# Kernel optimization log

Measured on AMD Instinct MI355X. Metric: run time of the kernel, lower is better.

Reference implementation:

```python
import jax, jax.numpy as jnp
import numpy as np

N_ATOMS = 6144
BOX = 40.0  # Angstrom, simulation box edge


def setup_inputs() -> dict:
    key = jax.random.key(0)
    k1, k2 = jax.random.split(key)
    coordinates = jax.random.uniform(k1, (1, N_ATOMS, 3), dtype=jnp.float32) * BOX
    species = jax.random.randint(k2, (1, N_ATOMS), 0, 4)  # no -1 dummy atoms
    return {"species": species, "coordinates": coordinates, "cutoff": 5}


def reference(species, coordinates, cutoff):
    # Faithful math of CellList.forward with pbc=None (no PBC):
    # the grid/bucket pipeline only accelerates finding all (i, j), i > j
    # pairs with |r_i - r_j| <= cutoff (tril_indices ordering), excluding
    # dummy atoms (species == -1). Output: dense masked distance map where
    # entry [i, j] = distance if pair is a screened neighbor else 0.
    coords = coordinates.reshape(-1, 3)
    n = coords.shape[0]
    cutoff = jnp.float32(cutoff)
    diff = coords[:, None, :] - coords[None, :, :]           # [N, N, 3] = r_i - r_j
    sq = jnp.sum(diff * diff, axis=-1)                       # [N, N]
    dist = jnp.sqrt(jnp.where(sq > 0, sq, 1.0))              # safe sqrt (diag sq==0)
    dummy = species.reshape(-1) == -1
    valid = jnp.tril(jnp.ones((n, n), dtype=bool), k=-1)     # i > j, as tril_indices(offset=-1)
    valid = valid & (~dummy[:, None]) & (~dummy[None, :])
    # screening uses detached coords in the original -> mask is non-diff anyway
    mask = valid & (dist <= cutoff) & (sq > 0)
    return jnp.where(mask, dist, 0.0)
```

## Files before the change

kernel.cpp:

```cpp
#include <hip/hip_runtime.h>
#include <math.h>


constexpr int N     = 6144;
constexpr int CPT   = 8;
constexpr int BLOCK = 256;
constexpr int CPB   = BLOCK * CPT;

template <bool ICHECK>
__device__ __forceinline__ void compute_strip(
    const float* __restrict__ coords, const int* __restrict__ species,
    float T, int i, int j0, float* __restrict__ outp)
{
    const float xi = coords[3 * i + 0];
    const float yi = coords[3 * i + 1];
    const float zi = coords[3 * i + 2];

    const float4* cj = reinterpret_cast<const float4*>(coords + 3 * (size_t)j0);
    float f[24];
#pragma unroll
    for (int q = 0; q < 6; ++q) {
        const float4 v = cj[q];
        f[4 * q + 0] = v.x; f[4 * q + 1] = v.y;
        f[4 * q + 2] = v.z; f[4 * q + 3] = v.w;
    }
    const int4 sa = *reinterpret_cast<const int4*>(species + j0);
    const int4 sb = *reinterpret_cast<const int4*>(species + j0 + 4);
    const int sj[8] = {sa.x, sa.y, sa.z, sa.w, sb.x, sb.y, sb.z, sb.w};

    float r[8];
#pragma unroll
    for (int k = 0; k < 8; ++k) {
        const float dx = __fsub_rn(xi, f[3 * k + 0]);
        const float dy = __fsub_rn(yi, f[3 * k + 1]);
        const float dz = __fsub_rn(zi, f[3 * k + 2]);
        const float sq = __fadd_rn(__fadd_rn(__fmul_rn(dx, dx), __fmul_rn(dy, dy)),
                                   __fmul_rn(dz, dz));
        bool m = (sq <= T) && (sj[k] != -1);
        if (ICHECK) m = m && (j0 + k < i);
        r[k] = m ? __builtin_amdgcn_sqrtf(sq) : 0.0f;
    }
    float4* ov = reinterpret_cast<float4*>(outp);
    ov[0] = make_float4(r[0], r[1], r[2], r[3]);
    ov[1] = make_float4(r[4], r[5], r[6], r[7]);
}

__global__ __launch_bounds__(BLOCK) void cell_list_kernel(
    const float* __restrict__ coords,
    const int*   __restrict__ species,
    const int*   __restrict__ cutoff_p,
    float*       __restrict__ out)
{
    const int i    = blockIdx.y;
    const int base = blockIdx.x * CPB;
    const int j0   = base + (int)threadIdx.x * CPT;
    float* outp = out + (size_t)i * N + j0;

    const int si = species[i];
    if (i <= base || si == -1) {
        const float4 z = make_float4(0.f, 0.f, 0.f, 0.f);
        float4* ov = reinterpret_cast<float4*>(outp);
        ov[0] = z; ov[1] = z;
        return;
    }

    const float  c  = (float)cutoff_p[0];
    const float  cn = __int_as_float(__float_as_int(c) + 1);
    const double md = (double)c + 0.5 * ((double)cn - (double)c);
    const double Td = md * md;
    float T = (float)Td;
    if ((double)T > Td) T = __int_as_float(__float_as_int(T) - 1);

    if (base + CPB <= i)
        compute_strip<false>(coords, species, T, i, j0, outp);
    else
        compute_strip<true>(coords, species, T, i, j0, outp);
}

extern "C" void kernel_launch(void* const* d_in, const int* in_sizes, int n_in,
                              void* d_out, int out_size, void* d_ws, size_t ws_size,
                              hipStream_t stream) {
    const int*   species = (const int*)d_in[0];
    const float* coords  = (const float*)d_in[1];
    const int*   cutoff  = (const int*)d_in[2];
    float*       out     = (float*)d_out;

    dim3 block(BLOCK);
    dim3 grid(N / CPB, N);
    hipLaunchKernelGGL(cell_list_kernel, grid, block, 0, stream,
                       coords, species, cutoff, out);
}
```

Before: 162.2 us.

## Process six rows per block reusing j-coordinates with nontemporal stores

Each block now handles six consecutive output rows for one column strip. It loads the j-coordinates and species into registers once and reuses them across those rows, and it uses a 1D grid. Output writes switch to nontemporal stores to avoid polluting cache with the 151MB write stream. The kernel is store-bandwidth bound, so the gain depends mostly on store efficiency, while fewer blocks may reduce latency hiding.

```diff
diff --git a/kernel.cpp b/kernel.cpp
--- a/kernel.cpp
+++ b/kernel.cpp
@@ -2,48 +2,15 @@
 #include <math.h>
 
 
-constexpr int N     = 6144;
-constexpr int CPT   = 8;
-constexpr int BLOCK = 256;
-constexpr int CPB   = BLOCK * CPT;
+typedef float v4f __attribute__((ext_vector_type(4)));
 
-template <bool ICHECK>
-__device__ __forceinline__ void compute_strip(
-    const float* __restrict__ coords, const int* __restrict__ species,
-    float T, int i, int j0, float* __restrict__ outp)
-{
-    const float xi = coords[3 * i + 0];
-    const float yi = coords[3 * i + 1];
-    const float zi = coords[3 * i + 2];
-
-    const float4* cj = reinterpret_cast<const float4*>(coords + 3 * (size_t)j0);
-    float f[24];
-#pragma unroll
-    for (int q = 0; q < 6; ++q) {
-        const float4 v = cj[q];
-        f[4 * q + 0] = v.x; f[4 * q + 1] = v.y;
-        f[4 * q + 2] = v.z; f[4 * q + 3] = v.w;
-    }
-    const int4 sa = *reinterpret_cast<const int4*>(species + j0);
-    const int4 sb = *reinterpret_cast<const int4*>(species + j0 + 4);
-    const int sj[8] = {sa.x, sa.y, sa.z, sa.w, sb.x, sb.y, sb.z, sb.w};
-
-    float r[8];
-#pragma unroll
-    for (int k = 0; k < 8; ++k) {
-        const float dx = __fsub_rn(xi, f[3 * k + 0]);
-        const float dy = __fsub_rn(yi, f[3 * k + 1]);
-        const float dz = __fsub_rn(zi, f[3 * k + 2]);
-        const float sq = __fadd_rn(__fadd_rn(__fmul_rn(dx, dx), __fmul_rn(dy, dy)),
-                                   __fmul_rn(dz, dz));
-        bool m = (sq <= T) && (sj[k] != -1);
-        if (ICHECK) m = m && (j0 + k < i);
-        r[k] = m ? __builtin_amdgcn_sqrtf(sq) : 0.0f;
-    }
-    float4* ov = reinterpret_cast<float4*>(outp);
-    ov[0] = make_float4(r[0], r[1], r[2], r[3]);
-    ov[1] = make_float4(r[4], r[5], r[6], r[7]);
-}
+constexpr int N      = 6144;
+constexpr int CPT    = 8;
+constexpr int BLOCK  = 256;
+constexpr int CPB    = BLOCK * CPT;
+constexpr int NSTRIP = N / CPB;
+constexpr int RPB    = 6;
+constexpr int NROWG  = N / RPB;
 
 __global__ __launch_bounds__(BLOCK) void cell_list_kernel(
     const float* __restrict__ coords,
@@ -51,18 +18,11 @@
     const int*   __restrict__ cutoff_p,
     float*       __restrict__ out)
 {
-    const int i    = blockIdx.y;
-    const int base = blockIdx.x * CPB;
-    const int j0   = base + (int)threadIdx.x * CPT;
-    float* outp = out + (size_t)i * N + j0;
-
-    const int si = species[i];
-    if (i <= base || si == -1) {
-        const float4 z = make_float4(0.f, 0.f, 0.f, 0.f);
-        float4* ov = reinterpret_cast<float4*>(outp);
-        ov[0] = z; ov[1] = z;
-        return;
-    }
+    const int bx    = blockIdx.x;
+    const int strip = bx % NSTRIP;
+    const int i0    = (bx / NSTRIP) * RPB;
+    const int base  = strip * CPB;
+    const int j0    = base + (int)threadIdx.x * CPT;
 
     const float  c  = (float)cutoff_p[0];
     const float  cn = __int_as_float(__float_as_int(c) + 1);
@@ -71,10 +31,56 @@
     float T = (float)Td;
     if ((double)T > Td) T = __int_as_float(__float_as_int(T) - 1);
 
-    if (base + CPB <= i)
-        compute_strip<false>(coords, species, T, i, j0, outp);
-    else
-        compute_strip<true>(coords, species, T, i, j0, outp);
+    float f[24];
+    int   sj[8];
+    if (i0 + RPB - 1 > base) {
+        const float4* cj = reinterpret_cast<const float4*>(coords + 3 * (size_t)j0);
+#pragma unroll
+        for (int q = 0; q < 6; ++q) {
+            const float4 v = cj[q];
+            f[4 * q + 0] = v.x; f[4 * q + 1] = v.y;
+            f[4 * q + 2] = v.z; f[4 * q + 3] = v.w;
+        }
+        const int4 sa = *reinterpret_cast<const int4*>(species + j0);
+        const int4 sb = *reinterpret_cast<const int4*>(species + j0 + 4);
+        sj[0] = sa.x; sj[1] = sa.y; sj[2] = sa.z; sj[3] = sa.w;
+        sj[4] = sb.x; sj[5] = sb.y; sj[6] = sb.z; sj[7] = sb.w;
+    }
+
+    const v4f zero4 = {0.f, 0.f, 0.f, 0.f};
+
+    for (int rr = 0; rr < RPB; ++rr) {
+        const int i = i0 + rr;
+        v4f* ov = reinterpret_cast<v4f*>(out + (size_t)i * N + j0);
+        const int si = species[i];
+
+        if (i <= base || si == -1) {
+            __builtin_nontemporal_store(zero4, ov + 0);
+            __builtin_nontemporal_store(zero4, ov + 1);
+            continue;
+        }
+
+        const float xi = coords[3 * i + 0];
+        const float yi = coords[3 * i + 1];
+        const float zi = coords[3 * i + 2];
+
+        float r[8];
+#pragma unroll
+        for (int k = 0; k < 8; ++k) {
+            const float dx = __fsub_rn(xi, f[3 * k + 0]);
+            const float dy = __fsub_rn(yi, f[3 * k + 1]);
+            const float dz = __fsub_rn(zi, f[3 * k + 2]);
+            const float sq = __fadd_rn(
+                __fadd_rn(__fmul_rn(dx, dx), __fmul_rn(dy, dy)),
+                __fmul_rn(dz, dz));
+            const bool m = (sq <= T) && (sj[k] != -1) && (j0 + k < i);
+            r[k] = m ? __builtin_amdgcn_sqrtf(sq) : 0.0f;
+        }
+        const v4f lo = {r[0], r[1], r[2], r[3]};
+        const v4f hi = {r[4], r[5], r[6], r[7]};
+        __builtin_nontemporal_store(lo, ov + 0);
+        __builtin_nontemporal_store(hi, ov + 1);
+    }
 }
 
 extern "C" void kernel_launch(void* const* d_in, const int* in_sizes, int n_in,
@@ -86,7 +92,7 @@
     float*       out     = (float*)d_out;
 
     dim3 block(BLOCK);
-    dim3 grid(N / CPB, N);
+    dim3 grid(NSTRIP * NROWG);
     hipLaunchKernelGGL(cell_list_kernel, grid, block, 0, stream,
                        coords, species, cutoff, out);
 }
```

Result: slower. 192.7 us (+18.8%).
